# Performance work log

Hardware: AMD Instinct MI355X
Metric: run time of the kernel (lower is better)

Reference implementation:

```python
import jax, jax.numpy as jnp
import numpy as np

N, D = 8192, 512
NUM_SOURCES = 8


def setup_inputs() -> dict:
    key = jax.random.key(0)
    k1, k2, k3 = jax.random.split(key, 3)
    image_features = jax.random.normal(k1, (N, D), dtype=jnp.float32)
    text_features = jax.random.normal(k2, (N, D), dtype=jnp.float32)
    logit_scale = jnp.ones((), dtype=jnp.float32)
    source_labels = jax.random.randint(k3, (N,), 0, NUM_SOURCES, dtype=jnp.int64)
    return {
        "image_features": image_features,
        "text_features": text_features,
        "logit_scale": logit_scale,
        "source_labels": source_labels,
    }


def reference(image_features, text_features, logit_scale, source_labels):
    n = source_labels.shape[0]
    # [N, N] logits and row-wise log-softmax
    logits = logit_scale * (image_features @ text_features.T)
    log_probs = jax.nn.log_softmax(logits, axis=1)
    # same-source mask, diagonal excluded
    mask = (source_labels[:, None] == source_labels[None, :]) & (~jnp.eye(n, dtype=bool))
    count_pos = mask.sum(axis=1)  # [N]
    row_sum = jnp.where(mask, log_probs, 0.0).sum(axis=1)  # [N]
    # per-row mean over positives; rows with zero positives contribute 0
    row_mean = jnp.where(count_pos > 0, row_sum / jnp.maximum(count_pos, 1).astype(log_probs.dtype), 0.0)
    # loss = -(sum_i row_mean_i) / N
    return -row_mean.sum() / n
```

## Files before the change

kernel.cpp:

```cpp
#include <hip/hip_runtime.h>
#include <cmath>

#define NN 8192
#define DD 512
#define NSRC 8
#define SPLITS 16
#define BM 128
#define BN 128
#define BK 64
#define CPS (NN / SPLITS)
#define CTILES (CPS / BN)
#define COFF 100.0f

typedef __bf16 bf16x8 __attribute__((ext_vector_type(8)));
typedef float  f32x4  __attribute__((ext_vector_type(4)));

__device__ __forceinline__ unsigned short f2bf(float f) {
    unsigned u = __float_as_uint(f);
    u += 0x7fffu + ((u >> 16) & 1u);
    return (unsigned short)(u >> 16);
}

__global__ __launch_bounds__(256) void k_cast(
    const float* __restrict__ img, const float* __restrict__ txt,
    unsigned short* __restrict__ imgB, unsigned short* __restrict__ txtB,
    float* __restrict__ Tsum, int* __restrict__ counts, float* __restrict__ out)
{
    if (blockIdx.x == 0) {
        float4 z = {0.f, 0.f, 0.f, 0.f};
#pragma unroll
        for (int k = 0; k < 4; k++)
            *(float4*)(Tsum + (k * 256 + threadIdx.x) * 4) = z;
        if (threadIdx.x < NSRC) counts[threadIdx.x] = 0;
        if (threadIdx.x == 0) out[0] = 0.f;
    }
    const size_t gid = (size_t)blockIdx.x * 256 + threadIdx.x;
    const size_t half = (size_t)NN * DD / 8;
    const float* src = (gid < half) ? img : txt;
    unsigned short* dst = (gid < half) ? imgB : txtB;
    const size_t off = ((gid < half) ? gid : gid - half) * 8;
    const float4 v0 = *(const float4*)(src + off);
    const float4 v1 = *(const float4*)(src + off + 4);
    union { unsigned short s[8]; uint4 v; } o;
    o.s[0] = f2bf(v0.x); o.s[1] = f2bf(v0.y); o.s[2] = f2bf(v0.z); o.s[3] = f2bf(v0.w);
    o.s[4] = f2bf(v1.x); o.s[5] = f2bf(v1.y); o.s[6] = f2bf(v1.z); o.s[7] = f2bf(v1.w);
    *(uint4*)(dst + off) = o.v;
}

__global__ __launch_bounds__(256) void k_src_sums(
    const float* __restrict__ txt, const int* __restrict__ labels,
    float* __restrict__ Tsum, int* __restrict__ counts)
{
    __shared__ float Tacc[NSRC * DD];
    __shared__ int cacc[NSRC];
    const int tid = threadIdx.x;
    const int d0 = 2 * tid;
#pragma unroll
    for (int s = 0; s < NSRC; s++) {
        Tacc[s * DD + d0] = 0.f;
        Tacc[s * DD + d0 + 1] = 0.f;
    }
    if (tid < NSRC) cacc[tid] = 0;
    __syncthreads();

    const int row0 = blockIdx.x * 64;
    if (tid < 64) atomicAdd(&cacc[labels[row0 + tid]], 1);

    for (int j = 0; j < 64; j++) {
        const int lab = labels[row0 + j];
        const float2 v = *(const float2*)(txt + (size_t)(row0 + j) * DD + d0);
        Tacc[lab * DD + d0]     += v.x;
        Tacc[lab * DD + d0 + 1] += v.y;
    }
    __syncthreads();
#pragma unroll
    for (int k = 0; k < NSRC * DD / 256; k++) {
        const int e = k * 256 + tid;
        atomicAdd(&Tsum[e], Tacc[e]);
    }
    if (tid < NSRC) atomicAdd(&counts[tid], cacc[tid]);
}

__global__ __launch_bounds__(256) void k_lse_mfma(
    const unsigned short* __restrict__ imgB, const unsigned short* __restrict__ txtB,
    const float* __restrict__ scale_p,
    float* __restrict__ ps)
{
    __shared__ uint4 lds[2048];
    const float scale = scale_p[0];
    const int tid  = threadIdx.x;
    const int lane = tid & 63;
    const int w    = tid >> 6;
    const int split = blockIdx.x & (SPLITS - 1);
    const int by    = blockIdx.x / SPLITS;
    const int row0  = by * BM;
    const int colBase = split * CPS;
    const int lq = lane >> 4;
    const int ln = lane & 15;

    int st_r[4], st_kc[4];
#pragma unroll
    for (int t = 0; t < 4; t++) {
        const int p = t * 256 + tid;
        st_r[t]  = p >> 3;
        st_kc[t] = (p & 7) ^ (st_r[t] & 7);
    }

    int aIdx[2], aSw[2], bIdx[8], bSw[8];
#pragma unroll
    for (int i = 0; i < 2; i++) {
        const int r = w * 32 + i * 16 + ln;
        aIdx[i] = r * 8; aSw[i] = r & 7;
    }
#pragma unroll
    for (int j = 0; j < 8; j++) {
        const int r = j * 16 + ln;
        bIdx[j] = 1024 + r * 8; bSw[j] = r & 7;
    }

    float s_run[2][4];
#pragma unroll
    for (int i = 0; i < 2; i++)
#pragma unroll
        for (int rg = 0; rg < 4; rg++) s_run[i][rg] = 0.f;

    for (int ct = 0; ct < CTILES; ct++) {
        const int col0 = colBase + ct * BN;
        f32x4 acc[2][8];
#pragma unroll
        for (int i = 0; i < 2; i++)
#pragma unroll
            for (int j = 0; j < 8; j++) acc[i][j] = (f32x4){0.f, 0.f, 0.f, 0.f};

        for (int kt = 0; kt < DD; kt += BK) {
            __syncthreads();
#pragma unroll
            for (int t = 0; t < 4; t++) {
                const unsigned short* g =
                    imgB + (size_t)(row0 + st_r[t]) * DD + kt + (st_kc[t] << 3);
                __builtin_amdgcn_global_load_lds(
                    (const __attribute__((address_space(1))) void*)g,
                    (__attribute__((address_space(3))) void*)&lds[t * 256 + (w << 6)],
                    16, 0, 0);
            }
#pragma unroll
            for (int t = 0; t < 4; t++) {
                const unsigned short* g =
                    txtB + (size_t)(col0 + st_r[t]) * DD + kt + (st_kc[t] << 3);
                __builtin_amdgcn_global_load_lds(
                    (const __attribute__((address_space(1))) void*)g,
                    (__attribute__((address_space(3))) void*)&lds[1024 + t * 256 + (w << 6)],
                    16, 0, 0);
            }
            __syncthreads();
#pragma unroll
            for (int ks = 0; ks < 2; ks++) {
                bf16x8 af[2], bf[8];
#pragma unroll
                for (int i = 0; i < 2; i++)
                    af[i] = *reinterpret_cast<const bf16x8*>(
                        &lds[aIdx[i] + (((ks << 2) + lq) ^ aSw[i])]);
#pragma unroll
                for (int j = 0; j < 8; j++)
                    bf[j] = *reinterpret_cast<const bf16x8*>(
                        &lds[bIdx[j] + (((ks << 2) + lq) ^ bSw[j])]);
#pragma unroll
                for (int i = 0; i < 2; i++)
#pragma unroll
                    for (int j = 0; j < 8; j++)
                        acc[i][j] = __builtin_amdgcn_mfma_f32_16x16x32_bf16(
                            af[i], bf[j], acc[i][j], 0, 0, 0);
            }
        }
#pragma unroll
        for (int i = 0; i < 2; i++)
#pragma unroll
        for (int rg = 0; rg < 4; rg++) {
            float es = s_run[i][rg];
#pragma unroll
            for (int j = 0; j < 8; j++)
                es += __expf(fmaf(acc[i][j][rg], scale, -COFF));
            s_run[i][rg] = es;
        }
    }
#pragma unroll
    for (int i = 0; i < 2; i++)
#pragma unroll
    for (int rg = 0; rg < 4; rg++) {
        float es = s_run[i][rg];
#pragma unroll
        for (int off = 8; off; off >>= 1) es += __shfl_xor(es, off);
        s_run[i][rg] = es;
    }
    if (ln == 0) {
#pragma unroll
        for (int i = 0; i < 2; i++)
#pragma unroll
        for (int rg = 0; rg < 4; rg++) {
            const int row = row0 + w * 32 + i * 16 + lq * 4 + rg;
            ps[(size_t)row * SPLITS + split] = s_run[i][rg];
        }
    }
}

__global__ __launch_bounds__(256) void k_finalize(
    const float* __restrict__ img, const float* __restrict__ txt,
    const int* __restrict__ labels, const float* __restrict__ scale_p,
    const float* __restrict__ Tsum, const int* __restrict__ counts,
    const float* __restrict__ ps,
    float* __restrict__ out)
{
    const float scale = scale_p[0];
    const int tid = threadIdx.x;
    const int lane = tid & 63;
    const int wave = tid >> 6;
    const int rowBase = blockIdx.x * 16 + wave * 4;
    float local = 0.f;
#pragma unroll
    for (int it = 0; it < 4; it++) {
        const int i = rowBase + it;
        const int lab = labels[i];
        float ds = 0.f, dt = 0.f;
        const float* ip = img + (size_t)i * DD;
        const float* tp = txt + (size_t)i * DD;
        const float* sp = Tsum + lab * DD;
#pragma unroll
        for (int k = lane; k < DD; k += 64) {
            const float a = ip[k];
            ds = fmaf(a, tp[k], ds);
            dt = fmaf(a, sp[k], dt);
        }
#pragma unroll
        for (int off = 32; off; off >>= 1) {
            ds += __shfl_xor(ds, off);
            dt += __shfl_xor(dt, off);
        }
        if (lane == 0) {
            float ssum = 0.f;
#pragma unroll
            for (int s = 0; s < SPLITS; s++)
                ssum += ps[(size_t)i * SPLITS + s];
            const float lse = COFF + __logf(ssum);
            const int cnt = counts[lab] - 1;
            if (cnt > 0) {
                const float row_sum = scale * (dt - ds) - (float)cnt * lse;
                local += row_sum / (float)cnt;
            }
        }
    }
    __shared__ float red[4];
    if (lane == 0) red[wave] = local;
    __syncthreads();
    if (tid == 0) {
        const float t = red[0] + red[1] + red[2] + red[3];
        atomicAdd(out, -t / (float)NN);
    }
}

extern "C" void kernel_launch(void* const* d_in, const int* in_sizes, int n_in,
                              void* d_out, int out_size, void* d_ws, size_t ws_size,
                              hipStream_t stream)
{
    const float* img     = (const float*)d_in[0];
    const float* txt     = (const float*)d_in[1];
    const float* scale_p = (const float*)d_in[2];
    const int*   labels  = (const int*)d_in[3];
    float* out = (float*)d_out;

    char* ws = (char*)d_ws;
    float* ps    = (float*)(ws);
    float* Tsum  = (float*)(ws + (size_t)NN * SPLITS * 4);
    int*   counts = (int*)(ws + (size_t)NN * SPLITS * 4 + NSRC * DD * 4);
    unsigned short* imgB = (unsigned short*)(ws + 2 * 1024 * 1024);
    unsigned short* txtB = (unsigned short*)(ws + 10 * 1024 * 1024);

    k_cast<<<(2 * NN * DD / 8) / 256, 256, 0, stream>>>(img, txt, imgB, txtB,
                                                        Tsum, counts, out);
    k_src_sums<<<NN / 64, 256, 0, stream>>>(txt, labels, Tsum, counts);
    k_lse_mfma<<<(NN / BM) * SPLITS, 256, 0, stream>>>(imgB, txtB, scale_p, ps);
    k_finalize<<<NN / 16, 256, 0, stream>>>(img, txt, labels, scale_p,
                                            Tsum, counts, ps, out);
}
```

Measured before the change: 186.4 us.

## Rewrite LSE GEMM as 256x256-tile, 8-wave, double-buffered pipelined MFMA kernel

```diff
diff --git a/kernel.cpp b/kernel.cpp
--- a/kernel.cpp
+++ b/kernel.cpp
@@ -4,12 +4,7 @@
 #define NN 8192
 #define DD 512
 #define NSRC 8
-#define SPLITS 16
-#define BM 128
-#define BN 128
-#define BK 64
-#define CPS (NN / SPLITS)
-#define CTILES (CPS / BN)
+#define PSW 32
 #define COFF 100.0f
 
 typedef __bf16 bf16x8 __attribute__((ext_vector_type(8)));
@@ -81,126 +76,147 @@
     if (tid < NSRC) atomicAdd(&counts[tid], cacc[tid]);
 }
 
-__global__ __launch_bounds__(256) void k_lse_mfma(
+__global__ __launch_bounds__(512, 2) void k_lse_mfma256(
     const unsigned short* __restrict__ imgB, const unsigned short* __restrict__ txtB,
-    const float* __restrict__ scale_p,
-    float* __restrict__ ps)
-{
-    __shared__ uint4 lds[2048];
+    const float* __restrict__ scale_p, float* __restrict__ ps)
+{
+    __shared__ uint4 lds[8192];
     const float scale = scale_p[0];
     const int tid  = threadIdx.x;
     const int lane = tid & 63;
     const int w    = tid >> 6;
-    const int split = blockIdx.x & (SPLITS - 1);
-    const int by    = blockIdx.x / SPLITS;
-    const int row0  = by * BM;
-    const int colBase = split * CPS;
-    const int lq = lane >> 4;
-    const int ln = lane & 15;
-
-    int st_r[4], st_kc[4];
-#pragma unroll
-    for (int t = 0; t < 4; t++) {
-        const int p = t * 256 + tid;
-        st_r[t]  = p >> 3;
-        st_kc[t] = (p & 7) ^ (st_r[t] & 7);
-    }
-
-    int aIdx[2], aSw[2], bIdx[8], bSw[8];
-#pragma unroll
-    for (int i = 0; i < 2; i++) {
-        const int r = w * 32 + i * 16 + ln;
-        aIdx[i] = r * 8; aSw[i] = r & 7;
-    }
-#pragma unroll
-    for (int j = 0; j < 8; j++) {
-        const int r = j * 16 + ln;
-        bIdx[j] = 1024 + r * 8; bSw[j] = r & 7;
-    }
-
-    float s_run[2][4];
-#pragma unroll
-    for (int i = 0; i < 2; i++)
-#pragma unroll
-        for (int rg = 0; rg < 4; rg++) s_run[i][rg] = 0.f;
-
-    for (int ct = 0; ct < CTILES; ct++) {
-        const int col0 = colBase + ct * BN;
-        f32x4 acc[2][8];
-#pragma unroll
-        for (int i = 0; i < 2; i++)
-#pragma unroll
-            for (int j = 0; j < 8; j++) acc[i][j] = (f32x4){0.f, 0.f, 0.f, 0.f};
-
-        for (int kt = 0; kt < DD; kt += BK) {
-            __syncthreads();
-#pragma unroll
-            for (int t = 0; t < 4; t++) {
-                const unsigned short* g =
-                    imgB + (size_t)(row0 + st_r[t]) * DD + kt + (st_kc[t] << 3);
-                __builtin_amdgcn_global_load_lds(
-                    (const __attribute__((address_space(1))) void*)g,
-                    (__attribute__((address_space(3))) void*)&lds[t * 256 + (w << 6)],
-                    16, 0, 0);
-            }
-#pragma unroll
-            for (int t = 0; t < 4; t++) {
-                const unsigned short* g =
-                    txtB + (size_t)(col0 + st_r[t]) * DD + kt + (st_kc[t] << 3);
-                __builtin_amdgcn_global_load_lds(
-                    (const __attribute__((address_space(1))) void*)g,
-                    (__attribute__((address_space(3))) void*)&lds[1024 + t * 256 + (w << 6)],
-                    16, 0, 0);
-            }
-            __syncthreads();
-#pragma unroll
-            for (int ks = 0; ks < 2; ks++) {
-                bf16x8 af[2], bf[8];
-#pragma unroll
-                for (int i = 0; i < 2; i++)
-                    af[i] = *reinterpret_cast<const bf16x8*>(
-                        &lds[aIdx[i] + (((ks << 2) + lq) ^ aSw[i])]);
-#pragma unroll
-                for (int j = 0; j < 8; j++)
-                    bf[j] = *reinterpret_cast<const bf16x8*>(
-                        &lds[bIdx[j] + (((ks << 2) + lq) ^ bSw[j])]);
-#pragma unroll
-                for (int i = 0; i < 2; i++)
-#pragma unroll
-                    for (int j = 0; j < 8; j++)
-                        acc[i][j] = __builtin_amdgcn_mfma_f32_16x16x32_bf16(
-                            af[i], bf[j], acc[i][j], 0, 0, 0);
-            }
-        }
-#pragma unroll
-        for (int i = 0; i < 2; i++)
+    const int wr   = w >> 2;
+    const int wc   = w & 3;
+    const int lq   = lane >> 4;
+    const int ln   = lane & 15;
+    const int by   = blockIdx.x >> 5;
+    const int bcol = blockIdx.x & 31;
+    const int row0 = by * 256;
+    const int col0 = bcol * 256;
+
+    const int st_r  = tid >> 3;
+    const int st_kc = (tid & 7) ^ (st_r & 7);
+    const int xsw   = ln & 7;
+
+    int rowA[2][4], colB[2][2];
+#pragma unroll
+    for (int ih = 0; ih < 2; ih++)
+#pragma unroll
+        for (int ii = 0; ii < 4; ii++)
+            rowA[ih][ii] = (wr * 128 + ih * 64 + ii * 16 + ln) * 8;
+#pragma unroll
+    for (int jh = 0; jh < 2; jh++)
+#pragma unroll
+        for (int jj = 0; jj < 2; jj++)
+            colB[jh][jj] = (wc * 64 + jh * 32 + jj * 16 + ln) * 8;
+
+#define SA(BUF, Q, T)                                                          \
+    { const unsigned short* g = imgB + (size_t)(row0 + (Q) * 64 + st_r) * DD   \
+          + (((T) & 7) << 6) + (st_kc << 3);                                   \
+      __builtin_amdgcn_global_load_lds(                                        \
+          (const __attribute__((address_space(1))) void*)g,                    \
+          (__attribute__((address_space(3))) void*)                            \
+              &lds[(BUF) * 4096 + (Q) * 512 + tid], 16, 0, 0); }
+#define SB(BUF, Q, T)                                                          \
+    { const unsigned short* g = txtB + (size_t)(col0 + (Q) * 64 + st_r) * DD   \
+          + (((T) & 7) << 6) + (st_kc << 3);                                   \
+      __builtin_amdgcn_global_load_lds(                                        \
+          (const __attribute__((address_space(1))) void*)g,                    \
+          (__attribute__((address_space(3))) void*)                            \
+              &lds[(BUF) * 4096 + 2048 + (Q) * 512 + tid], 16, 0, 0); }
+
+#define PHASE_(BUF, IH, JH, RA, STG, VM)                                       \
+    do {                                                                       \
+        if (RA) {                                                              \
+            _Pragma("unroll") for (int ii = 0; ii < 4; ii++) {                 \
+                _Pragma("unroll") for (int ks = 0; ks < 2; ks++) {             \
+                    af[ii][ks] = *reinterpret_cast<const bf16x8*>(             \
+                        &lds[(BUF) * 4096 + rowA[IH][ii]                       \
+                             + (((ks << 2) + lq) ^ xsw)]);                     \
+                }                                                              \
+            }                                                                  \
+        }                                                                      \
+        bf16x8 bf[2][2];                                                       \
+        _Pragma("unroll") for (int jj = 0; jj < 2; jj++) {                     \
+            _Pragma("unroll") for (int ks = 0; ks < 2; ks++) {                 \
+                bf[jj][ks] = *reinterpret_cast<const bf16x8*>(                 \
+                    &lds[(BUF) * 4096 + 2048 + colB[JH][jj]                    \
+                         + (((ks << 2) + lq) ^ xsw)]);                         \
+            }                                                                  \
+        }                                                                      \
+        STG;                                                                   \
+        __builtin_amdgcn_s_barrier();                                          \
+        asm volatile("s_waitcnt lgkmcnt(0)" ::: "memory");                     \
+        __builtin_amdgcn_sched_barrier(0);                                     \
+        __builtin_amdgcn_s_setprio(1);                                         \
+        _Pragma("unroll") for (int ks = 0; ks < 2; ks++) {                     \
+            _Pragma("unroll") for (int ii = 0; ii < 4; ii++) {                 \
+                _Pragma("unroll") for (int jj = 0; jj < 2; jj++) {             \
+                    acc[(IH) * 4 + ii][(JH) * 2 + jj] =                        \
+                        __builtin_amdgcn_mfma_f32_16x16x32_bf16(               \
+                            af[ii][ks], bf[jj][ks],                            \
+                            acc[(IH) * 4 + ii][(JH) * 2 + jj], 0, 0, 0);       \
+                }                                                              \
+            }                                                                  \
+        }                                                                      \
+        __builtin_amdgcn_s_setprio(0);                                         \
+        if (VM) { asm volatile("s_waitcnt vmcnt(2)" ::: "memory"); }           \
+        __builtin_amdgcn_s_barrier();                                          \
+    } while (0)
+
+#pragma unroll
+    for (int q = 0; q < 4; q++) SA(0, q, 0);
+#pragma unroll
+    for (int q = 0; q < 4; q++) SB(0, q, 0);
+    SA(1, 0, 1); SA(1, 2, 1);
+    asm volatile("s_waitcnt vmcnt(2)" ::: "memory");
+    __builtin_amdgcn_s_barrier();
+
+    f32x4 acc[8][4];
+#pragma unroll
+    for (int i = 0; i < 8; i++)
+#pragma unroll
+        for (int j = 0; j < 4; j++) acc[i][j] = (f32x4){0.f, 0.f, 0.f, 0.f};
+    bf16x8 af[4][2];
+
+    for (int t0 = 0; t0 < DD / 64; t0 += 2) {
+        PHASE_(0, 0, 0, 1, SA(1, 1, t0 + 1); SA(1, 3, t0 + 1), 0);
+        PHASE_(0, 0, 1, 0, SB(1, 0, t0 + 1); SB(1, 1, t0 + 1), 0);
+        PHASE_(0, 1, 0, 1, SB(1, 2, t0 + 1); SB(1, 3, t0 + 1), 0);
+        PHASE_(0, 1, 1, 0, SA(0, 0, t0 + 2); SA(0, 2, t0 + 2), 1);
+        PHASE_(1, 0, 0, 1, SA(0, 1, t0 + 2); SA(0, 3, t0 + 2), 0);
+        PHASE_(1, 0, 1, 0, SB(0, 0, t0 + 2); SB(0, 1, t0 + 2), 0);
+        PHASE_(1, 1, 0, 1, SB(0, 2, t0 + 2); SB(0, 3, t0 + 2), 0);
+        PHASE_(1, 1, 1, 0, SA(1, 0, t0 + 3); SA(1, 2, t0 + 3), 1);
+    }
+
+    asm volatile("s_waitcnt vmcnt(0)" ::: "memory");
+    __syncthreads();
+
+    float* fred = (float*)lds;
+#pragma unroll
+    for (int i = 0; i < 8; i++) {
 #pragma unroll
         for (int rg = 0; rg < 4; rg++) {
-            float es = s_run[i][rg];
-#pragma unroll
-            for (int j = 0; j < 8; j++)
+            float es = 0.f;
+#pragma unroll
+            for (int j = 0; j < 4; j++)
                 es += __expf(fmaf(acc[i][j][rg], scale, -COFF));
-            s_run[i][rg] = es;
-        }
-    }
-#pragma unroll
-    for (int i = 0; i < 2; i++)
-#pragma unroll
-    for (int rg = 0; rg < 4; rg++) {
-        float es = s_run[i][rg];
-#pragma unroll
-        for (int off = 8; off; off >>= 1) es += __shfl_xor(es, off);
-        s_run[i][rg] = es;
-    }
-    if (ln == 0) {
-#pragma unroll
-        for (int i = 0; i < 2; i++)
-#pragma unroll
-        for (int rg = 0; rg < 4; rg++) {
-            const int row = row0 + w * 32 + i * 16 + lq * 4 + rg;
-            ps[(size_t)row * SPLITS + split] = s_run[i][rg];
-        }
-    }
+#pragma unroll
+            for (int off = 8; off; off >>= 1) es += __shfl_xor(es, off);
+            if (ln == 0)
+                fred[(wr * 128 + i * 16 + lq * 4 + rg) * 4 + wc] = es;
+        }
+    }
+    __syncthreads();
+    if (tid < 256) {
+        const float tot = fred[tid * 4] + fred[tid * 4 + 1]
+                        + fred[tid * 4 + 2] + fred[tid * 4 + 3];
+        ps[(size_t)(row0 + tid) * PSW + bcol] = tot;
+    }
+#undef SA
+#undef SB
+#undef PHASE_
 }
 
 __global__ __launch_bounds__(256) void k_finalize(
@@ -230,17 +246,15 @@
             ds = fmaf(a, tp[k], ds);
             dt = fmaf(a, sp[k], dt);
         }
+        float es = (lane < PSW) ? ps[(size_t)i * PSW + lane] : 0.f;
 #pragma unroll
         for (int off = 32; off; off >>= 1) {
             ds += __shfl_xor(ds, off);
             dt += __shfl_xor(dt, off);
+            es += __shfl_xor(es, off);
         }
         if (lane == 0) {
-            float ssum = 0.f;
-#pragma unroll
-            for (int s = 0; s < SPLITS; s++)
-                ssum += ps[(size_t)i * SPLITS + s];
-            const float lse = COFF + __logf(ssum);
+            const float lse = COFF + __logf(es);
             const int cnt = counts[lab] - 1;
             if (cnt > 0) {
                 const float row_sum = scale * (dt - ds) - (float)cnt * lse;
@@ -269,15 +283,16 @@
 
     char* ws = (char*)d_ws;
     float* ps    = (float*)(ws);
-    float* Tsum  = (float*)(ws + (size_t)NN * SPLITS * 4);
-    int*   counts = (int*)(ws + (size_t)NN * SPLITS * 4 + NSRC * DD * 4);
+    float* Tsum  = (float*)(ws + (1 << 20));
+    int*   counts = (int*)(ws + (1 << 20) + NSRC * DD * 4);
     unsigned short* imgB = (unsigned short*)(ws + 2 * 1024 * 1024);
     unsigned short* txtB = (unsigned short*)(ws + 10 * 1024 * 1024);
 
     k_cast<<<(2 * NN * DD / 8) / 256, 256, 0, stream>>>(img, txt, imgB, txtB,
                                                         Tsum, counts, out);
     k_src_sums<<<NN / 64, 256, 0, stream>>>(txt, labels, Tsum, counts);
-    k_lse_mfma<<<(NN / BM) * SPLITS, 256, 0, stream>>>(imgB, txtB, scale_p, ps);
+    k_lse_mfma256<<<(NN / 256) * (NN / 256), 512, 0, stream>>>(imgB, txtB,
+                                                               scale_p, ps);
     k_finalize<<<NN / 16, 256, 0, stream>>>(img, txt, labels, scale_p,
                                             Tsum, counts, ps, out);
 }
```

Result: faster. 180.2 us (-3.4%).
